# Optimization experiments

Measured on AMD Instinct MI355X. Metric: run time of the kernel, lower is better.

## Reference

```python
import jax, jax.numpy as jnp
import numpy as np

SEQLEN = np.array([1024, 768, 512, 1536, 256, 1280, 512, 1024], dtype=np.int32)
HIDDEN = 2048
HEAD_NUM = 16


def setup_inputs() -> dict:
    key = jax.random.key(0)
    k1, k2 = jax.random.split(key)
    total = int(SEQLEN.sum())
    a = jax.random.normal(k1, (total, HIDDEN), dtype=jnp.float32) * 0.02
    b = jax.random.normal(k2, (total, HIDDEN), dtype=jnp.float32) * 0.02
    return {"a": a, "b": b, "seqlen": np.asarray(SEQLEN), "head_num": HEAD_NUM}


def reference(a, b, seqlen, head_num):
    # Variable-length strided batched matmul (QK^T), no padding.
    # a, b: [sum(seqlen), hidden]; output: flat concat of per-seq [head_num, s, s].
    seqlen = np.asarray(seqlen)
    offs = np.concatenate([[0], np.cumsum(seqlen)])  # static offsets
    hidden = a.shape[1]
    head_size = hidden // head_num
    outs = []
    for i, s in enumerate(seqlen.tolist()):
        ai = a[offs[i]:offs[i + 1]].reshape(s, head_num, head_size)
        bi = b[offs[i]:offs[i + 1]].reshape(s, head_num, head_size)
        # per-head QK^T: [head_num, s, s]
        ci = jnp.einsum('shd,thd->hst', ai, bi)
        outs.append(ci.reshape(-1))
    return jnp.concatenate(outs)
```

## Files before the change

### kernel.cpp

```cpp
#include <hip/hip_runtime.h>

#define NSEQ   8
#define HEADS  16
#define HSIZE  128
#define HIDDEN 2048
#define BT     128
#define LDS_PAD 8
#define LDS_ROW (HSIZE + LDS_PAD)

typedef __attribute__((ext_vector_type(8))) short  bf16x8;
typedef __attribute__((ext_vector_type(4))) float  f32x4;

struct SeqMap {
    int       s[NSEQ];
    int       row_off[NSEQ];
    long long out_off[NSEQ];
    int       t[NSEQ];
    int       blk_start[NSEQ];
    int       nblk;
};

__device__ __forceinline__ unsigned short f2bf(float x) {
    unsigned int u = __builtin_bit_cast(unsigned int, x);
    u += 0x7fffu + ((u >> 16) & 1u);
    return (unsigned short)(u >> 16);
}

__global__ __launch_bounds__(256, 2) void qkt_strip_kernel(
    const float* __restrict__ A, const float* __restrict__ B,
    float* __restrict__ out, SeqMap map)
{
    __shared__ unsigned short lds[2][BT * LDS_ROW];

    const int cpx = map.nblk >> 3;
    const int bid = ((int)blockIdx.x % 8) * cpx + ((int)blockIdx.x / 8);

    int i = 0;
    #pragma unroll
    for (int k = 1; k < NSEQ; ++k) if (bid >= map.blk_start[k]) i = k;
    const int local = bid - map.blk_start[i];
    const int t     = map.t[i];
    const int h     = local / t;
    const int tr    = local - h * t;
    const int s     = map.s[i];
    const int row0  = map.row_off[i];

    const int tid  = threadIdx.x;
    const int r0   = tid >> 5;
    const int c4   = tid & 31;
    const size_t hcol = (size_t)h * HSIZE + (size_t)c4 * 4;

    const int lane = tid & 63;
    const int w    = tid >> 6;
    const int wr   = w >> 1;
    const int wc   = w & 1;
    const int lrow = lane & 15;
    const int kgrp = lane >> 4;

    unsigned short* ldsw0 = &lds[0][r0 * LDS_ROW + c4 * 4];
    unsigned short* ldsw1 = &lds[1][r0 * LDS_ROW + c4 * 4];

    {
        const float* sa = A + (size_t)(row0 + tr * BT + r0) * HIDDEN + hcol;
        const float* sb = B + (size_t)(row0 + r0) * HIDDEN + hcol;
        float4 ga[16], gb[16];
        #pragma unroll
        for (int it = 0; it < 16; ++it) ga[it] = *(const float4*)(sa + (size_t)it * 8 * HIDDEN);
        #pragma unroll
        for (int it = 0; it < 16; ++it) gb[it] = *(const float4*)(sb + (size_t)it * 8 * HIDDEN);
        #pragma unroll
        for (int it = 0; it < 16; ++it) {
            ushort4 p; p.x=f2bf(ga[it].x); p.y=f2bf(ga[it].y); p.z=f2bf(ga[it].z); p.w=f2bf(ga[it].w);
            *(ushort4*)(ldsw0 + it * 8 * LDS_ROW) = p;
        }
        #pragma unroll
        for (int it = 0; it < 16; ++it) {
            ushort4 p; p.x=f2bf(gb[it].x); p.y=f2bf(gb[it].y); p.z=f2bf(gb[it].z); p.w=f2bf(gb[it].w);
            *(ushort4*)(ldsw1 + it * 8 * LDS_ROW) = p;
        }
    }
    __syncthreads();

    bf16x8 af[4][4];
    #pragma unroll
    for (int m = 0; m < 4; ++m)
        #pragma unroll
        for (int kk = 0; kk < 4; ++kk)
            af[m][kk] = *(const bf16x8*)&lds[0][(wr*64 + m*16 + lrow) * LDS_ROW + kk*32 + kgrp*8];
    __syncthreads();

    int cur = 1;
    const long long obase = map.out_off[i] + (long long)h * s * s;
    float* orow = out + obase
                + (long long)(tr * BT + wr * 64 + lrow) * s
                + (wc * 64 + kgrp * 4);
    const long long s16 = (long long)s * 16;

    const float* sbnext = B + (size_t)(row0 + BT + r0) * HIDDEN + hcol;

    for (int tc = 0; tc < t; ++tc) {
        const bool has_next = (tc + 1 < t);

        float4 g[16];
        if (has_next) {
            #pragma unroll
            for (int it = 0; it < 16; ++it) g[it] = *(const float4*)(sbnext + (size_t)it * 8 * HIDDEN);
        }

        f32x4 acc[4][4];
        #pragma unroll
        for (int m = 0; m < 4; ++m)
            #pragma unroll
            for (int n = 0; n < 4; ++n)
                acc[m][n] = (f32x4){0.f, 0.f, 0.f, 0.f};

        const unsigned short* lb = &lds[cur][0];
        #pragma unroll
        for (int kk = 0; kk < 4; ++kk) {
            bf16x8 bfr[4];
            #pragma unroll
            for (int n = 0; n < 4; ++n)
                bfr[n] = *(const bf16x8*)&lb[(wc*64 + n*16 + lrow) * LDS_ROW + kk*32 + kgrp*8];
            #pragma unroll
            for (int m = 0; m < 4; ++m)
                #pragma unroll
                for (int n = 0; n < 4; ++n)
                    acc[m][n] = __builtin_amdgcn_mfma_f32_16x16x32_bf16(
                                    bfr[n], af[m][kk], acc[m][n], 0, 0, 0);
        }

        {
            float* op = orow + tc * BT;
            #pragma unroll
            for (int m = 0; m < 4; ++m)
                #pragma unroll
                for (int n = 0; n < 4; ++n)
                    __builtin_nontemporal_store(acc[m][n],
                        (f32x4*)(op + (long long)m * s16 + n * 16));
        }

        if (has_next) {
            unsigned short* dst = cur ? ldsw0 : ldsw1;
            #pragma unroll
            for (int it = 0; it < 16; ++it) {
                ushort4 p; p.x=f2bf(g[it].x); p.y=f2bf(g[it].y); p.z=f2bf(g[it].z); p.w=f2bf(g[it].w);
                *(ushort4*)(dst + it * 8 * LDS_ROW) = p;
            }
            sbnext += (size_t)BT * HIDDEN;
        }

        if (has_next) {
            __builtin_amdgcn_sched_barrier(0);
            asm volatile("s_waitcnt lgkmcnt(0)" ::: "memory");
            __builtin_amdgcn_s_barrier();
            __builtin_amdgcn_sched_barrier(0);
        }
        cur ^= 1;
    }
}

extern "C" void kernel_launch(void* const* d_in, const int* in_sizes, int n_in,
                              void* d_out, int out_size, void* d_ws, size_t ws_size,
                              hipStream_t stream) {
    const float* A = (const float*)d_in[0];
    const float* B = (const float*)d_in[1];
    float* out = (float*)d_out;

    static const int S[NSEQ] = {1024, 768, 512, 1536, 256, 1280, 512, 1024};

    int row_off[NSEQ]; long long out_off[NSEQ];
    int row = 0; long long o = 0;
    for (int i = 0; i < NSEQ; ++i) {
        row_off[i] = row; out_off[i] = o;
        row += S[i];
        o   += (long long)HEADS * S[i] * S[i];
    }

    static const int order[NSEQ] = {3, 5, 0, 7, 1, 2, 6, 4};

    SeqMap map;
    int blk = 0;
    for (int k = 0; k < NSEQ; ++k) {
        const int i = order[k];
        const int t = S[i] / BT;
        map.s[k]         = S[i];
        map.row_off[k]   = row_off[i];
        map.out_off[k]   = out_off[i];
        map.t[k]         = t;
        map.blk_start[k] = blk;
        blk += HEADS * t;
    }
    map.nblk = blk;

    qkt_strip_kernel<<<blk, 256, 0, stream>>>(A, B, out, map);
}
```

Baseline: 187.1 us.

## Prefetch B tiles two steps ahead and switch to normal output stores

Restructures the strip loop into a deeper software pipeline. Global loads of B run two tiles ahead in registers, while the previously loaded tile is converted and written to the other LDS buffer before the MFMA work. The A and B prologue now shares one register array to cut register pressure. Output stores change from nontemporal to normal stores, and the sched_barrier fences are removed, which gives the compiler more freedom but may weaken the intended overlap.

```diff
diff --git a/kernel.cpp b/kernel.cpp
--- a/kernel.cpp
+++ b/kernel.cpp
@@ -26,7 +26,13 @@
     return (unsigned short)(u >> 16);
 }
 
-__global__ __launch_bounds__(256, 2) void qkt_strip_kernel(
+__device__ __forceinline__ ushort4 f2bf4(float4 v) {
+    ushort4 p;
+    p.x = f2bf(v.x); p.y = f2bf(v.y); p.z = f2bf(v.z); p.w = f2bf(v.w);
+    return p;
+}
+
+__global__ __launch_bounds__(256, 2) void qkt_pipe_kernel(
     const float* __restrict__ A, const float* __restrict__ B,
     float* __restrict__ out, SeqMap map)
 {
@@ -60,24 +66,15 @@
     unsigned short* ldsw0 = &lds[0][r0 * LDS_ROW + c4 * 4];
     unsigned short* ldsw1 = &lds[1][r0 * LDS_ROW + c4 * 4];
 
+    float4 g[16];
+
     {
         const float* sa = A + (size_t)(row0 + tr * BT + r0) * HIDDEN + hcol;
-        const float* sb = B + (size_t)(row0 + r0) * HIDDEN + hcol;
-        float4 ga[16], gb[16];
-        #pragma unroll
-        for (int it = 0; it < 16; ++it) ga[it] = *(const float4*)(sa + (size_t)it * 8 * HIDDEN);
-        #pragma unroll
-        for (int it = 0; it < 16; ++it) gb[it] = *(const float4*)(sb + (size_t)it * 8 * HIDDEN);
-        #pragma unroll
-        for (int it = 0; it < 16; ++it) {
-            ushort4 p; p.x=f2bf(ga[it].x); p.y=f2bf(ga[it].y); p.z=f2bf(ga[it].z); p.w=f2bf(ga[it].w);
-            *(ushort4*)(ldsw0 + it * 8 * LDS_ROW) = p;
-        }
-        #pragma unroll
-        for (int it = 0; it < 16; ++it) {
-            ushort4 p; p.x=f2bf(gb[it].x); p.y=f2bf(gb[it].y); p.z=f2bf(gb[it].z); p.w=f2bf(gb[it].w);
-            *(ushort4*)(ldsw1 + it * 8 * LDS_ROW) = p;
-        }
+        #pragma unroll
+        for (int it = 0; it < 16; ++it) g[it] = *(const float4*)(sa + (size_t)it * 8 * HIDDEN);
+        #pragma unroll
+        for (int it = 0; it < 16; ++it)
+            *(ushort4*)(ldsw0 + it * 8 * LDS_ROW) = f2bf4(g[it]);
     }
     __syncthreads();
 
@@ -89,22 +86,42 @@
             af[m][kk] = *(const bf16x8*)&lds[0][(wr*64 + m*16 + lrow) * LDS_ROW + kk*32 + kgrp*8];
     __syncthreads();
 
-    int cur = 1;
+    {
+        const float* sb = B + (size_t)(row0 + r0) * HIDDEN + hcol;
+        #pragma unroll
+        for (int it = 0; it < 16; ++it) g[it] = *(const float4*)(sb + (size_t)it * 8 * HIDDEN);
+        #pragma unroll
+        for (int it = 0; it < 16; ++it)
+            *(ushort4*)(ldsw0 + it * 8 * LDS_ROW) = f2bf4(g[it]);
+    }
+    if (t > 1) {
+        const float* sb = B + (size_t)(row0 + BT + r0) * HIDDEN + hcol;
+        #pragma unroll
+        for (int it = 0; it < 16; ++it) g[it] = *(const float4*)(sb + (size_t)it * 8 * HIDDEN);
+    }
+    __syncthreads();
+
+    int cur = 0;
     const long long obase = map.out_off[i] + (long long)h * s * s;
     float* orow = out + obase
                 + (long long)(tr * BT + wr * 64 + lrow) * s
                 + (wc * 64 + kgrp * 4);
     const long long s16 = (long long)s * 16;
 
-    const float* sbnext = B + (size_t)(row0 + BT + r0) * HIDDEN + hcol;
+    const float* sbpre = B + (size_t)(row0 + 2 * BT + r0) * HIDDEN + hcol;
 
     for (int tc = 0; tc < t; ++tc) {
-        const bool has_next = (tc + 1 < t);
-
-        float4 g[16];
-        if (has_next) {
-            #pragma unroll
-            for (int it = 0; it < 16; ++it) g[it] = *(const float4*)(sbnext + (size_t)it * 8 * HIDDEN);
+        if (tc + 1 < t) {
+            unsigned short* dst = cur ? ldsw0 : ldsw1;
+            #pragma unroll
+            for (int it = 0; it < 16; ++it)
+                *(ushort4*)(dst + it * 8 * LDS_ROW) = f2bf4(g[it]);
+        }
+
+        if (tc + 2 < t) {
+            #pragma unroll
+            for (int it = 0; it < 16; ++it) g[it] = *(const float4*)(sbpre + (size_t)it * 8 * HIDDEN);
+            sbpre += (size_t)BT * HIDDEN;
         }
 
         f32x4 acc[4][4];
@@ -135,25 +152,12 @@
             for (int m = 0; m < 4; ++m)
                 #pragma unroll
                 for (int n = 0; n < 4; ++n)
-                    __builtin_nontemporal_store(acc[m][n],
-                        (f32x4*)(op + (long long)m * s16 + n * 16));
-        }
-
-        if (has_next) {
-            unsigned short* dst = cur ? ldsw0 : ldsw1;
-            #pragma unroll
-            for (int it = 0; it < 16; ++it) {
-                ushort4 p; p.x=f2bf(g[it].x); p.y=f2bf(g[it].y); p.z=f2bf(g[it].z); p.w=f2bf(g[it].w);
-                *(ushort4*)(dst + it * 8 * LDS_ROW) = p;
-            }
-            sbnext += (size_t)BT * HIDDEN;
-        }
-
-        if (has_next) {
-            __builtin_amdgcn_sched_barrier(0);
+                    *(f32x4*)(op + (long long)m * s16 + n * 16) = acc[m][n];
+        }
+
+        if (tc + 1 < t) {
             asm volatile("s_waitcnt lgkmcnt(0)" ::: "memory");
             __builtin_amdgcn_s_barrier();
-            __builtin_amdgcn_sched_barrier(0);
         }
         cur ^= 1;
     }
@@ -192,5 +196,5 @@
     }
     map.nblk = blk;
 
-    qkt_strip_kernel<<<blk, 256, 0, stream>>>(A, B, out, map);
-}
+    qkt_pipe_kernel<<<blk, 256, 0, stream>>>(A, B, out, map);
+}
```

New measurement: 211.0 us. 1.13x slower.
